# Optimization experiments

Measured on AMD Instinct MI355X. Metric: run time of the kernel, lower is better.

## Reference

```python
import jax, jax.numpy as jnp
import numpy as np

EMBED = 512
HEADS = 8
HEAD_DIM = EMBED // HEADS


def setup_inputs() -> dict:
    key = jax.random.key(0)
    ks = jax.random.split(key, 12)
    B, L, D = 2, 4096, EMBED
    s = 1.0 / np.sqrt(D)  # torch Linear default init range scale (approx, uniform)
    def lin(k):
        kw, kb = jax.random.split(k)
        W = jax.random.uniform(kw, (D, D), jnp.float32, -s, s)
        b = jax.random.uniform(kb, (D,), jnp.float32, -s, s)
        return W, b
    Wq, bq = lin(ks[0])
    Wk, bk = lin(ks[1])
    Wv, bv = lin(ks[2])
    Wo, bo = lin(ks[3])
    query = jax.random.normal(ks[4], (B, L, D), jnp.float32)
    key_t = jax.random.normal(ks[5], (B, L, D), jnp.float32)
    value = jax.random.normal(ks[6], (B, L, D), jnp.float32)
    return {"query": query, "key": key_t, "value": value,
            "Wq": Wq, "bq": bq, "Wk": Wk, "bk": bk,
            "Wv": Wv, "bv": bv, "Wo": Wo, "bo": bo}


def reference(query, key, value, Wq, bq, Wk, bk, Wv, bv, Wo, bo):
    B, L, D = query.shape
    H, Hd = HEADS, HEAD_DIM
    scale = Hd ** -0.5
    # torch nn.Linear: y = x @ W.T + b
    q = (query @ Wq.T + bq).reshape(B, L, H, Hd).transpose(0, 2, 1, 3)   # [B,H,L,Hd]
    k = (key   @ Wk.T + bk).reshape(B, -1, H, Hd).transpose(0, 2, 1, 3)
    v = (value @ Wv.T + bv).reshape(B, -1, H, Hd).transpose(0, 2, 1, 3)
    scores = jnp.einsum('bhqd,bhkd->bhqk', q, k) * scale                  # [B,H,L,L]
    causal = jnp.triu(jnp.ones((L, L), dtype=bool), k=1)                  # True above diag
    neg = jnp.finfo(scores.dtype).min
    scores = jnp.where(causal, neg, scores)
    attn = jax.nn.softmax(scores, axis=-1)
    # dropout is identity in eval mode
    out = jnp.einsum('bhqk,bhkd->bhqd', attn, v)                          # [B,H,L,Hd]
    out = out.transpose(0, 2, 1, 3).reshape(B, L, D)
    return out @ Wo.T + bo, attn
```

## Files before the change

kernel.cpp:

```cpp
#include <hip/hip_runtime.h>
#include <hip/hip_bf16.h>


typedef __attribute__((ext_vector_type(8))) __bf16 bf16x8;
typedef __attribute__((ext_vector_type(4))) float f32x4;

constexpr int LL = 4096;
constexpr int DD = 512;
constexpr int HH = 8;
constexpr int HD = 64;
constexpr int BB = 2;
constexpr int BL = BB * LL;
constexpr size_t OUT_ELEMS = (size_t)BB * LL * DD;

static __device__ inline bf16x8 cvt8(const float* p) {
    float4 a = *reinterpret_cast<const float4*>(p);
    float4 b = *reinterpret_cast<const float4*>(p + 4);
    bf16x8 r;
    r[0] = (__bf16)a.x; r[1] = (__bf16)a.y; r[2] = (__bf16)a.z; r[3] = (__bf16)a.w;
    r[4] = (__bf16)b.x; r[5] = (__bf16)b.y; r[6] = (__bf16)b.z; r[7] = (__bf16)b.w;
    return r;
}

__global__ __launch_bounds__(256) void qkv_kernel(
    const float* __restrict__ q_in, const float* __restrict__ k_in,
    const float* __restrict__ v_in,
    const float* __restrict__ Wq, const float* __restrict__ bq,
    const float* __restrict__ Wk, const float* __restrict__ bk,
    const float* __restrict__ Wv, const float* __restrict__ bv,
    __bf16* __restrict__ Qb, __bf16* __restrict__ Kb, __bf16* __restrict__ Vt)
{
    const int z = blockIdx.z;
    const float* x   = (z == 0) ? q_in : (z == 1) ? k_in : v_in;
    const float* W   = (z == 0) ? Wq   : (z == 1) ? Wk   : Wv;
    const float* bia = (z == 0) ? bq   : (z == 1) ? bk   : bv;

    const int wid = threadIdx.x >> 6;
    const int lane = threadIdx.x & 63;
    const int l15 = lane & 15;
    const int lg  = lane >> 4;

    const int r0 = blockIdx.x * 64;
    const int c0 = blockIdx.y * 64 + wid * 16;

    f32x4 acc[4] = {};
    for (int k0 = 0; k0 < DD; k0 += 32) {
        bf16x8 bfrag = cvt8(&W[(size_t)(c0 + l15) * DD + k0 + lg * 8]);
#pragma unroll
        for (int mt = 0; mt < 4; ++mt) {
            bf16x8 afrag = cvt8(&x[(size_t)(r0 + mt * 16 + l15) * DD + k0 + lg * 8]);
            acc[mt] = __builtin_amdgcn_mfma_f32_16x16x32_bf16(afrag, bfrag, acc[mt], 0, 0, 0);
        }
    }

    const int col = c0 + l15;
    const float bval = bia[col];
    const int h = col >> 6, hd = col & 63;
#pragma unroll
    for (int mt = 0; mt < 4; ++mt) {
#pragma unroll
        for (int i = 0; i < 4; ++i) {
            const int row = r0 + mt * 16 + lg * 4 + i;
            const float val = acc[mt][i] + bval;
            const int b = row >> 12, l = row & (LL - 1);
            if (z == 2) {
                Vt[((size_t)(b * HH + h) * HD + hd) * LL + l] = (__bf16)val;
            } else {
                __bf16* dst = (z == 0) ? Qb : Kb;
                dst[((size_t)(b * HH + h) * LL + l) * HD + hd] = (__bf16)val;
            }
        }
    }
}

__global__ __launch_bounds__(256) void attn_kernel(
    const __bf16* __restrict__ Qb, const __bf16* __restrict__ Kb,
    const __bf16* __restrict__ Vt, __bf16* __restrict__ Ob,
    float* __restrict__ attn_out)
{
    const int qb = 63 - blockIdx.x;
    const int bh = blockIdx.y;

    const int wid = threadIdx.x >> 6;
    const int lane = threadIdx.x & 63;
    const int l15 = lane & 15;
    const int lg  = lane >> 4;

    const __bf16* Qh = Qb + (size_t)bh * LL * HD;
    const __bf16* Kh = Kb + (size_t)bh * LL * HD;
    const __bf16* Vh = Vt + (size_t)bh * HD * LL;
    float* A_out = attn_out + (size_t)bh * LL * LL;

    __shared__ float Pl[64][68];
    __shared__ float lred[4][64];
    __shared__ float linv_s[64];

    bf16x8 qf[4][2];
#pragma unroll
    for (int mt = 0; mt < 4; ++mt)
#pragma unroll
        for (int ks = 0; ks < 2; ++ks)
            qf[mt][ks] = *reinterpret_cast<const bf16x8*>(
                &Qh[(size_t)(qb * 64 + mt * 16 + l15) * HD + ks * 32 + lg * 8]);

    const float SC = 0.125f * 1.44269504088896f;

    float ps[16];
#pragma unroll
    for (int j = 0; j < 16; ++j) ps[j] = 0.f;

    for (int kb = 0; kb <= qb; ++kb) {
        f32x4 s[4] = {};
        const bf16x8 kf0 = *reinterpret_cast<const bf16x8*>(
            &Kh[(size_t)(kb * 64 + wid * 16 + l15) * HD + 0 + lg * 8]);
        const bf16x8 kf1 = *reinterpret_cast<const bf16x8*>(
            &Kh[(size_t)(kb * 64 + wid * 16 + l15) * HD + 32 + lg * 8]);
#pragma unroll
        for (int mt = 0; mt < 4; ++mt) {
            s[mt] = __builtin_amdgcn_mfma_f32_16x16x32_bf16(qf[mt][0], kf0, s[mt], 0, 0, 0);
            s[mt] = __builtin_amdgcn_mfma_f32_16x16x32_bf16(qf[mt][1], kf1, s[mt], 0, 0, 0);
        }
        if (kb == qb) {
            const int kcol = qb * 64 + wid * 16 + l15;
#pragma unroll
            for (int mt = 0; mt < 4; ++mt)
#pragma unroll
                for (int i = 0; i < 4; ++i) {
                    const int qrow = qb * 64 + mt * 16 + lg * 4 + i;
                    ps[mt * 4 + i] += (kcol <= qrow) ? exp2f(s[mt][i] * SC) : 0.f;
                }
        } else {
#pragma unroll
            for (int mt = 0; mt < 4; ++mt)
#pragma unroll
                for (int i = 0; i < 4; ++i)
                    ps[mt * 4 + i] += exp2f(s[mt][i] * SC);
        }
    }
#pragma unroll
    for (int off = 1; off < 16; off <<= 1)
#pragma unroll
        for (int j = 0; j < 16; ++j)
            ps[j] += __shfl_xor(ps[j], off, 64);
    if (l15 == 0) {
#pragma unroll
        for (int mt = 0; mt < 4; ++mt)
#pragma unroll
            for (int i = 0; i < 4; ++i)
                lred[wid][mt * 16 + lg * 4 + i] = ps[mt * 4 + i];
    }
    __syncthreads();
    if (threadIdx.x < 64)
        linv_s[threadIdx.x] = 1.0f / (lred[0][threadIdx.x] + lred[1][threadIdx.x] +
                                      lred[2][threadIdx.x] + lred[3][threadIdx.x]);
    __syncthreads();

    float li[16];
#pragma unroll
    for (int mt = 0; mt < 4; ++mt)
#pragma unroll
        for (int i = 0; i < 4; ++i)
            li[mt * 4 + i] = linv_s[mt * 16 + lg * 4 + i];

    f32x4 oacc[4] = {};
    const int tr = threadIdx.x >> 2;
    const int tc = threadIdx.x & 3;

    for (int kb = 0; kb <= qb; ++kb) {
        f32x4 s[4] = {};
        const bf16x8 kf0 = *reinterpret_cast<const bf16x8*>(
            &Kh[(size_t)(kb * 64 + wid * 16 + l15) * HD + 0 + lg * 8]);
        const bf16x8 kf1 = *reinterpret_cast<const bf16x8*>(
            &Kh[(size_t)(kb * 64 + wid * 16 + l15) * HD + 32 + lg * 8]);
#pragma unroll
        for (int mt = 0; mt < 4; ++mt) {
            s[mt] = __builtin_amdgcn_mfma_f32_16x16x32_bf16(qf[mt][0], kf0, s[mt], 0, 0, 0);
            s[mt] = __builtin_amdgcn_mfma_f32_16x16x32_bf16(qf[mt][1], kf1, s[mt], 0, 0, 0);
        }
        float pv[16];
        if (kb == qb) {
            const int kcol = qb * 64 + wid * 16 + l15;
#pragma unroll
            for (int mt = 0; mt < 4; ++mt)
#pragma unroll
                for (int i = 0; i < 4; ++i) {
                    const int qrow = qb * 64 + mt * 16 + lg * 4 + i;
                    pv[mt * 4 + i] = (kcol <= qrow)
                        ? exp2f(s[mt][i] * SC) * li[mt * 4 + i] : 0.f;
                }
        } else {
#pragma unroll
            for (int mt = 0; mt < 4; ++mt)
#pragma unroll
                for (int i = 0; i < 4; ++i)
                    pv[mt * 4 + i] = exp2f(s[mt][i] * SC) * li[mt * 4 + i];
        }

        __syncthreads();
#pragma unroll
        for (int mt = 0; mt < 4; ++mt)
#pragma unroll
            for (int i = 0; i < 4; ++i)
                Pl[mt * 16 + lg * 4 + i][wid * 16 + l15] = pv[mt * 4 + i];
        __syncthreads();

        {
            const size_t base = (size_t)(qb * 64 + tr) * LL + kb * 64 + tc * 16;
            float4* dst = reinterpret_cast<float4*>(&A_out[base]);
            const float* src = &Pl[tr][tc * 16];
            float4 v0 = *reinterpret_cast<const float4*>(src + 0);
            float4 v1 = *reinterpret_cast<const float4*>(src + 4);
            float4 v2 = *reinterpret_cast<const float4*>(src + 8);
            float4 v3 = *reinterpret_cast<const float4*>(src + 12);
            dst[0] = v0; dst[1] = v1; dst[2] = v2; dst[3] = v3;
        }

#pragma unroll
        for (int ks = 0; ks < 2; ++ks) {
            const bf16x8 vf = *reinterpret_cast<const bf16x8*>(
                &Vh[(size_t)(wid * 16 + l15) * LL + kb * 64 + ks * 32 + lg * 8]);
#pragma unroll
            for (int mt = 0; mt < 4; ++mt) {
                bf16x8 pa = cvt8(&Pl[mt * 16 + l15][ks * 32 + lg * 8]);
                oacc[mt] = __builtin_amdgcn_mfma_f32_16x16x32_bf16(pa, vf, oacc[mt], 0, 0, 0);
            }
        }
    }

    {
        const int b = bh >> 3, h = bh & 7;
        const int hd = wid * 16 + l15;
#pragma unroll
        for (int mt = 0; mt < 4; ++mt)
#pragma unroll
            for (int i = 0; i < 4; ++i) {
                const int ql = qb * 64 + mt * 16 + lg * 4 + i;
                Ob[(size_t)(b * LL + ql) * DD + h * HD + hd] = (__bf16)oacc[mt][i];
            }
    }

    {
        const int zstart = (qb + 1) * 64;
        const size_t rowbase = (size_t)(qb * 64 + tr) * LL;
        const float4 z4 = {0.f, 0.f, 0.f, 0.f};
        for (int c = zstart + tc * 16; c < LL; c += 64) {
            float4* dst = reinterpret_cast<float4*>(&A_out[rowbase + c]);
            dst[0] = z4; dst[1] = z4; dst[2] = z4; dst[3] = z4;
        }
    }
}

__global__ __launch_bounds__(256) void oproj_kernel(
    const __bf16* __restrict__ Ob, const float* __restrict__ Wo,
    const float* __restrict__ bo, float* __restrict__ out)
{
    const int wid = threadIdx.x >> 6;
    const int lane = threadIdx.x & 63;
    const int l15 = lane & 15;
    const int lg  = lane >> 4;

    const int r0 = blockIdx.x * 64;
    const int c0 = blockIdx.y * 64 + wid * 16;

    f32x4 acc[4] = {};
    for (int k0 = 0; k0 < DD; k0 += 32) {
        bf16x8 bfrag = cvt8(&Wo[(size_t)(c0 + l15) * DD + k0 + lg * 8]);
#pragma unroll
        for (int mt = 0; mt < 4; ++mt) {
            bf16x8 afrag = *reinterpret_cast<const bf16x8*>(
                &Ob[(size_t)(r0 + mt * 16 + l15) * DD + k0 + lg * 8]);
            acc[mt] = __builtin_amdgcn_mfma_f32_16x16x32_bf16(afrag, bfrag, acc[mt], 0, 0, 0);
        }
    }
    const float bval = bo[c0 + l15];
#pragma unroll
    for (int mt = 0; mt < 4; ++mt)
#pragma unroll
        for (int i = 0; i < 4; ++i)
            out[(size_t)(r0 + mt * 16 + lg * 4 + i) * DD + c0 + l15] = acc[mt][i] + bval;
}

extern "C" void kernel_launch(void* const* d_in, const int* in_sizes, int n_in,
                              void* d_out, int out_size, void* d_ws, size_t ws_size,
                              hipStream_t stream) {
    const float* query = (const float*)d_in[0];
    const float* key_t = (const float*)d_in[1];
    const float* value = (const float*)d_in[2];
    const float* Wq = (const float*)d_in[3];
    const float* bq = (const float*)d_in[4];
    const float* Wk = (const float*)d_in[5];
    const float* bk = (const float*)d_in[6];
    const float* Wv = (const float*)d_in[7];
    const float* bv = (const float*)d_in[8];
    const float* Wo = (const float*)d_in[9];
    const float* bo = (const float*)d_in[10];

    float* out  = (float*)d_out;
    float* attn = out + OUT_ELEMS;

    char* ws = (char*)d_ws;
    __bf16* Qb = (__bf16*)(ws);
    __bf16* Kb = (__bf16*)(ws + (size_t)8 * 1024 * 1024);
    __bf16* Vt = (__bf16*)(ws + (size_t)16 * 1024 * 1024);
    __bf16* Ob = (__bf16*)(ws + (size_t)24 * 1024 * 1024);

    qkv_kernel<<<dim3(BL / 64, DD / 64, 3), 256, 0, stream>>>(
        query, key_t, value, Wq, bq, Wk, bk, Wv, bv, Qb, Kb, Vt);
    attn_kernel<<<dim3(LL / 64, BB * HH), 256, 0, stream>>>(Qb, Kb, Vt, Ob, attn);
    oproj_kernel<<<dim3(BL / 64, DD / 64), 256, 0, stream>>>(Ob, Wo, bo, out);
}
```

Before: 833.7 us.

## Restructure attention so each warp owns query rows, dropping block barriers

```diff
diff --git a/kernel.cpp b/kernel.cpp
--- a/kernel.cpp
+++ b/kernel.cpp
@@ -19,6 +19,15 @@
     bf16x8 r;
     r[0] = (__bf16)a.x; r[1] = (__bf16)a.y; r[2] = (__bf16)a.z; r[3] = (__bf16)a.w;
     r[4] = (__bf16)b.x; r[5] = (__bf16)b.y; r[6] = (__bf16)b.z; r[7] = (__bf16)b.w;
+    return r;
+}
+
+static __device__ inline float4 up4(unsigned a, unsigned b) {
+    float4 r;
+    r.x = __uint_as_float(a << 16);
+    r.y = __uint_as_float(a & 0xffff0000u);
+    r.z = __uint_as_float(b << 16);
+    r.w = __uint_as_float(b & 0xffff0000u);
     return r;
 }
 
@@ -41,7 +50,8 @@
     const int lg  = lane >> 4;
 
     const int r0 = blockIdx.x * 64;
-    const int c0 = blockIdx.y * 64 + wid * 16;
+    const int cb = blockIdx.y;
+    const int c0 = cb * 64 + wid * 16;
 
     f32x4 acc[4] = {};
     for (int k0 = 0; k0 < DD; k0 += 32) {
@@ -53,23 +63,35 @@
         }
     }
 
-    const int col = c0 + l15;
-    const float bval = bia[col];
-    const int h = col >> 6, hd = col & 63;
-#pragma unroll
-    for (int mt = 0; mt < 4; ++mt) {
+    __shared__ __bf16 T[64][72];
+    const float bval = bia[c0 + l15];
+#pragma unroll
+    for (int mt = 0; mt < 4; ++mt)
 #pragma unroll
         for (int i = 0; i < 4; ++i) {
-            const int row = r0 + mt * 16 + lg * 4 + i;
             const float val = acc[mt][i] + bval;
-            const int b = row >> 12, l = row & (LL - 1);
-            if (z == 2) {
-                Vt[((size_t)(b * HH + h) * HD + hd) * LL + l] = (__bf16)val;
-            } else {
-                __bf16* dst = (z == 0) ? Qb : Kb;
-                dst[((size_t)(b * HH + h) * LL + l) * HD + hd] = (__bf16)val;
-            }
-        }
+            const int row = mt * 16 + lg * 4 + i;
+            const int col = wid * 16 + l15;
+            if (z == 2) T[col][row] = (__bf16)val;
+            else        T[row][col] = (__bf16)val;
+        }
+    __syncthreads();
+
+    const int tr  = threadIdx.x >> 2;
+    const int seg = threadIdx.x & 3;
+    uint4 v0 = *reinterpret_cast<const uint4*>(&T[tr][seg * 16]);
+    uint4 v1 = *reinterpret_cast<const uint4*>(&T[tr][seg * 16 + 8]);
+    const int b  = r0 >> 12;
+    const int l0 = r0 & (LL - 1);
+    if (z == 2) {
+        __bf16* dst = Vt + ((size_t)(b * HH + cb) * HD + tr) * LL + l0 + seg * 16;
+        *reinterpret_cast<uint4*>(dst)     = v0;
+        *reinterpret_cast<uint4*>(dst + 8) = v1;
+    } else {
+        __bf16* base = (z == 0) ? Qb : Kb;
+        __bf16* dst = base + ((size_t)(b * HH + cb) * LL + l0 + tr) * HD + seg * 16;
+        *reinterpret_cast<uint4*>(dst)     = v0;
+        *reinterpret_cast<uint4*>(dst + 8) = v1;
     }
 }
 
@@ -78,174 +100,143 @@
     const __bf16* __restrict__ Vt, __bf16* __restrict__ Ob,
     float* __restrict__ attn_out)
 {
-    const int qb = 63 - blockIdx.x;
-    const int bh = blockIdx.y;
-
-    const int wid = threadIdx.x >> 6;
+    const int bh = blockIdx.x;
+    const int qb = 63 - blockIdx.y;
+
+    const int w    = threadIdx.x >> 6;
     const int lane = threadIdx.x & 63;
-    const int l15 = lane & 15;
-    const int lg  = lane >> 4;
+    const int l15  = lane & 15;
+    const int lg   = lane >> 4;
 
     const __bf16* Qh = Qb + (size_t)bh * LL * HD;
     const __bf16* Kh = Kb + (size_t)bh * LL * HD;
     const __bf16* Vh = Vt + (size_t)bh * HD * LL;
     float* A_out = attn_out + (size_t)bh * LL * LL;
 
-    __shared__ float Pl[64][68];
-    __shared__ float lred[4][64];
-    __shared__ float linv_s[64];
-
-    bf16x8 qf[4][2];
-#pragma unroll
-    for (int mt = 0; mt < 4; ++mt)
-#pragma unroll
-        for (int ks = 0; ks < 2; ++ks)
-            qf[mt][ks] = *reinterpret_cast<const bf16x8*>(
-                &Qh[(size_t)(qb * 64 + mt * 16 + l15) * HD + ks * 32 + lg * 8]);
+    __shared__ __bf16 P[4][16][72];
+
+    const int q0 = qb * 64 + w * 16;
+    const bf16x8 qf0 = *reinterpret_cast<const bf16x8*>(&Qh[(size_t)(q0 + l15) * HD + lg * 8]);
+    const bf16x8 qf1 = *reinterpret_cast<const bf16x8*>(&Qh[(size_t)(q0 + l15) * HD + 32 + lg * 8]);
 
     const float SC = 0.125f * 1.44269504088896f;
 
-    float ps[16];
-#pragma unroll
-    for (int j = 0; j < 16; ++j) ps[j] = 0.f;
-
+    float rs[4] = {0.f, 0.f, 0.f, 0.f};
     for (int kb = 0; kb <= qb; ++kb) {
         f32x4 s[4] = {};
-        const bf16x8 kf0 = *reinterpret_cast<const bf16x8*>(
-            &Kh[(size_t)(kb * 64 + wid * 16 + l15) * HD + 0 + lg * 8]);
-        const bf16x8 kf1 = *reinterpret_cast<const bf16x8*>(
-            &Kh[(size_t)(kb * 64 + wid * 16 + l15) * HD + 32 + lg * 8]);
-#pragma unroll
-        for (int mt = 0; mt < 4; ++mt) {
-            s[mt] = __builtin_amdgcn_mfma_f32_16x16x32_bf16(qf[mt][0], kf0, s[mt], 0, 0, 0);
-            s[mt] = __builtin_amdgcn_mfma_f32_16x16x32_bf16(qf[mt][1], kf1, s[mt], 0, 0, 0);
+#pragma unroll
+        for (int kt = 0; kt < 4; ++kt) {
+            const __bf16* kp = &Kh[(size_t)(kb * 64 + kt * 16 + l15) * HD + lg * 8];
+            const bf16x8 k0 = *reinterpret_cast<const bf16x8*>(kp);
+            const bf16x8 k1 = *reinterpret_cast<const bf16x8*>(kp + 32);
+            s[kt] = __builtin_amdgcn_mfma_f32_16x16x32_bf16(qf0, k0, s[kt], 0, 0, 0);
+            s[kt] = __builtin_amdgcn_mfma_f32_16x16x32_bf16(qf1, k1, s[kt], 0, 0, 0);
         }
         if (kb == qb) {
-            const int kcol = qb * 64 + wid * 16 + l15;
-#pragma unroll
-            for (int mt = 0; mt < 4; ++mt)
+#pragma unroll
+            for (int kt = 0; kt < 4; ++kt)
 #pragma unroll
                 for (int i = 0; i < 4; ++i) {
-                    const int qrow = qb * 64 + mt * 16 + lg * 4 + i;
-                    ps[mt * 4 + i] += (kcol <= qrow) ? exp2f(s[mt][i] * SC) : 0.f;
+                    const int kcol = kb * 64 + kt * 16 + l15;
+                    const int qrow = q0 + lg * 4 + i;
+                    rs[i] += (kcol <= qrow) ? exp2f(s[kt][i] * SC) : 0.f;
                 }
         } else {
 #pragma unroll
-            for (int mt = 0; mt < 4; ++mt)
+            for (int kt = 0; kt < 4; ++kt)
 #pragma unroll
                 for (int i = 0; i < 4; ++i)
-                    ps[mt * 4 + i] += exp2f(s[mt][i] * SC);
+                    rs[i] += exp2f(s[kt][i] * SC);
         }
     }
 #pragma unroll
     for (int off = 1; off < 16; off <<= 1)
 #pragma unroll
-        for (int j = 0; j < 16; ++j)
-            ps[j] += __shfl_xor(ps[j], off, 64);
-    if (l15 == 0) {
-#pragma unroll
-        for (int mt = 0; mt < 4; ++mt)
-#pragma unroll
-            for (int i = 0; i < 4; ++i)
-                lred[wid][mt * 16 + lg * 4 + i] = ps[mt * 4 + i];
-    }
-    __syncthreads();
-    if (threadIdx.x < 64)
-        linv_s[threadIdx.x] = 1.0f / (lred[0][threadIdx.x] + lred[1][threadIdx.x] +
-                                      lred[2][threadIdx.x] + lred[3][threadIdx.x]);
-    __syncthreads();
-
-    float li[16];
-#pragma unroll
-    for (int mt = 0; mt < 4; ++mt)
-#pragma unroll
         for (int i = 0; i < 4; ++i)
-            li[mt * 4 + i] = linv_s[mt * 16 + lg * 4 + i];
+            rs[i] += __shfl_xor(rs[i], off, 64);
+    float llog[4];
+#pragma unroll
+    for (int i = 0; i < 4; ++i) llog[i] = -log2f(rs[i]);
 
     f32x4 oacc[4] = {};
-    const int tr = threadIdx.x >> 2;
-    const int tc = threadIdx.x & 3;
+    const int arow = lane >> 2;
+    const int aseg = lane & 3;
 
     for (int kb = 0; kb <= qb; ++kb) {
         f32x4 s[4] = {};
-        const bf16x8 kf0 = *reinterpret_cast<const bf16x8*>(
-            &Kh[(size_t)(kb * 64 + wid * 16 + l15) * HD + 0 + lg * 8]);
-        const bf16x8 kf1 = *reinterpret_cast<const bf16x8*>(
-            &Kh[(size_t)(kb * 64 + wid * 16 + l15) * HD + 32 + lg * 8]);
-#pragma unroll
-        for (int mt = 0; mt < 4; ++mt) {
-            s[mt] = __builtin_amdgcn_mfma_f32_16x16x32_bf16(qf[mt][0], kf0, s[mt], 0, 0, 0);
-            s[mt] = __builtin_amdgcn_mfma_f32_16x16x32_bf16(qf[mt][1], kf1, s[mt], 0, 0, 0);
-        }
-        float pv[16];
+#pragma unroll
+        for (int kt = 0; kt < 4; ++kt) {
+            const __bf16* kp = &Kh[(size_t)(kb * 64 + kt * 16 + l15) * HD + lg * 8];
+            const bf16x8 k0 = *reinterpret_cast<const bf16x8*>(kp);
+            const bf16x8 k1 = *reinterpret_cast<const bf16x8*>(kp + 32);
+            s[kt] = __builtin_amdgcn_mfma_f32_16x16x32_bf16(qf0, k0, s[kt], 0, 0, 0);
+            s[kt] = __builtin_amdgcn_mfma_f32_16x16x32_bf16(qf1, k1, s[kt], 0, 0, 0);
+        }
         if (kb == qb) {
-            const int kcol = qb * 64 + wid * 16 + l15;
-#pragma unroll
-            for (int mt = 0; mt < 4; ++mt)
+#pragma unroll
+            for (int kt = 0; kt < 4; ++kt)
 #pragma unroll
                 for (int i = 0; i < 4; ++i) {
-                    const int qrow = qb * 64 + mt * 16 + lg * 4 + i;
-                    pv[mt * 4 + i] = (kcol <= qrow)
-                        ? exp2f(s[mt][i] * SC) * li[mt * 4 + i] : 0.f;
+                    const int kcol = kb * 64 + kt * 16 + l15;
+                    const int qrow = q0 + lg * 4 + i;
+                    float e = exp2f(fmaf(s[kt][i], SC, llog[i]));
+                    if (kcol > qrow) e = 0.f;
+                    P[w][lg * 4 + i][kt * 16 + l15] = (__bf16)e;
                 }
         } else {
 #pragma unroll
-            for (int mt = 0; mt < 4; ++mt)
+            for (int kt = 0; kt < 4; ++kt)
 #pragma unroll
                 for (int i = 0; i < 4; ++i)
-                    pv[mt * 4 + i] = exp2f(s[mt][i] * SC) * li[mt * 4 + i];
-        }
-
-        __syncthreads();
-#pragma unroll
-        for (int mt = 0; mt < 4; ++mt)
+                    P[w][lg * 4 + i][kt * 16 + l15] =
+                        (__bf16)exp2f(fmaf(s[kt][i], SC, llog[i]));
+        }
+
+        {
+            uint4 a0 = *reinterpret_cast<const uint4*>(&P[w][arow][aseg * 16]);
+            uint4 a1 = *reinterpret_cast<const uint4*>(&P[w][arow][aseg * 16 + 8]);
+            float4* dst = reinterpret_cast<float4*>(
+                &A_out[(size_t)(q0 + arow) * LL + kb * 64 + aseg * 16]);
+            dst[0] = up4(a0.x, a0.y);
+            dst[1] = up4(a0.z, a0.w);
+            dst[2] = up4(a1.x, a1.y);
+            dst[3] = up4(a1.z, a1.w);
+        }
+
+        const bf16x8 pa0 = *reinterpret_cast<const bf16x8*>(&P[w][l15][lg * 8]);
+        const bf16x8 pa1 = *reinterpret_cast<const bf16x8*>(&P[w][l15][32 + lg * 8]);
+#pragma unroll
+        for (int ht = 0; ht < 4; ++ht) {
+            const __bf16* vp = &Vh[(size_t)(ht * 16 + l15) * LL + kb * 64 + lg * 8];
+            const bf16x8 vf0 = *reinterpret_cast<const bf16x8*>(vp);
+            const bf16x8 vf1 = *reinterpret_cast<const bf16x8*>(vp + 32);
+            oacc[ht] = __builtin_amdgcn_mfma_f32_16x16x32_bf16(pa0, vf0, oacc[ht], 0, 0, 0);
+            oacc[ht] = __builtin_amdgcn_mfma_f32_16x16x32_bf16(pa1, vf1, oacc[ht], 0, 0, 0);
+        }
+    }
+
+    {
+#pragma unroll
+        for (int ht = 0; ht < 4; ++ht)
 #pragma unroll
             for (int i = 0; i < 4; ++i)
-                Pl[mt * 16 + lg * 4 + i][wid * 16 + l15] = pv[mt * 4 + i];
-        __syncthreads();
-
-        {
-            const size_t base = (size_t)(qb * 64 + tr) * LL + kb * 64 + tc * 16;
-            float4* dst = reinterpret_cast<float4*>(&A_out[base]);
-            const float* src = &Pl[tr][tc * 16];
-            float4 v0 = *reinterpret_cast<const float4*>(src + 0);
-            float4 v1 = *reinterpret_cast<const float4*>(src + 4);
-            float4 v2 = *reinterpret_cast<const float4*>(src + 8);
-            float4 v3 = *reinterpret_cast<const float4*>(src + 12);
-            dst[0] = v0; dst[1] = v1; dst[2] = v2; dst[3] = v3;
-        }
-
-#pragma unroll
-        for (int ks = 0; ks < 2; ++ks) {
-            const bf16x8 vf = *reinterpret_cast<const bf16x8*>(
-                &Vh[(size_t)(wid * 16 + l15) * LL + kb * 64 + ks * 32 + lg * 8]);
-#pragma unroll
-            for (int mt = 0; mt < 4; ++mt) {
-                bf16x8 pa = cvt8(&Pl[mt * 16 + l15][ks * 32 + lg * 8]);
-                oacc[mt] = __builtin_amdgcn_mfma_f32_16x16x32_bf16(pa, vf, oacc[mt], 0, 0, 0);
-            }
-        }
+                P[w][lg * 4 + i][ht * 16 + l15] = (__bf16)oacc[ht][i];
+        uint4 o0 = *reinterpret_cast<const uint4*>(&P[w][arow][aseg * 16]);
+        uint4 o1 = *reinterpret_cast<const uint4*>(&P[w][arow][aseg * 16 + 8]);
+        const int b = bh >> 3, h = bh & 7;
+        __bf16* dst = Ob + ((size_t)(b * LL + q0 + arow)) * DD + h * HD + aseg * 16;
+        *reinterpret_cast<uint4*>(dst)     = o0;
+        *reinterpret_cast<uint4*>(dst + 8) = o1;
     }
 
     {
-        const int b = bh >> 3, h = bh & 7;
-        const int hd = wid * 16 + l15;
-#pragma unroll
-        for (int mt = 0; mt < 4; ++mt)
-#pragma unroll
-            for (int i = 0; i < 4; ++i) {
-                const int ql = qb * 64 + mt * 16 + lg * 4 + i;
-                Ob[(size_t)(b * LL + ql) * DD + h * HD + hd] = (__bf16)oacc[mt][i];
-            }
-    }
-
-    {
-        const int zstart = (qb + 1) * 64;
-        const size_t rowbase = (size_t)(qb * 64 + tr) * LL;
+        const int ztr = threadIdx.x >> 2;
+        const int zc  = (threadIdx.x & 3) * 16;
+        const size_t rowbase = (size_t)(qb * 64 + ztr) * LL;
         const float4 z4 = {0.f, 0.f, 0.f, 0.f};
-        for (int c = zstart + tc * 16; c < LL; c += 64) {
-            float4* dst = reinterpret_cast<float4*>(&A_out[rowbase + c]);
-            dst[0] = z4; dst[1] = z4; dst[2] = z4; dst[3] = z4;
+        for (int c = (qb + 1) * 64 + zc; c < LL; c += 64) {
+            float4* d = reinterpret_cast<float4*>(&A_out[rowbase + c]);
+            d[0] = z4; d[1] = z4; d[2] = z4; d[3] = z4;
         }
     }
 }
@@ -306,6 +297,6 @@
 
     qkv_kernel<<<dim3(BL / 64, DD / 64, 3), 256, 0, stream>>>(
         query, key_t, value, Wq, bq, Wk, bk, Wv, bv, Qb, Kb, Vt);
-    attn_kernel<<<dim3(LL / 64, BB * HH), 256, 0, stream>>>(Qb, Kb, Vt, Ob, attn);
+    attn_kernel<<<dim3(BB * HH, LL / 64), 256, 0, stream>>>(Qb, Kb, Vt, Ob, attn);
     oproj_kernel<<<dim3(BL / 64, DD / 64), 256, 0, stream>>>(Ob, Wo, bo, out);
 }
```

Result: slower. 901.3 us (+8.1%).
